# Kernel tuning notes

Measured on AMD Instinct MI355X. Metric: run time of the kernel, lower is better.

The kernel has to match this reference:

```python
import jax, jax.numpy as jnp
import numpy as np

DIM = 256
WIN = 7
HEADS = 8
N = WIN * WIN
HEAD_DIM = DIM // HEADS
SCALE = HEAD_DIM ** -0.5


def _relative_position_index():
    coords = np.stack(np.meshgrid(np.arange(WIN), np.arange(WIN), indexing='ij'))  # [2,W,W]
    cf = coords.reshape(2, -1)  # [2, N]
    rel = cf[:, :, None] - cf[:, None, :]  # [2, N, N]
    rel = rel.transpose(1, 2, 0)  # [N, N, 2]
    rel[:, :, 0] += WIN - 1
    rel[:, :, 1] += WIN - 1
    rel[:, :, 0] *= 2 * WIN - 1
    return rel.sum(-1).astype(np.int32)  # [N, N]


def setup_inputs() -> dict:
    key = jax.random.key(0)
    ks = jax.random.split(key, 8)
    B_ = 4096
    nW = 64
    x = jax.random.normal(ks[0], (B_, N, DIM), dtype=jnp.float32)
    mask = jnp.zeros((nW, N, N), dtype=jnp.float32)
    qkv_w = jax.random.normal(ks[1], (3 * DIM, DIM), dtype=jnp.float32) * (DIM ** -0.5)
    qkv_b = jnp.zeros((3 * DIM,), dtype=jnp.float32)
    proj_w = jax.random.normal(ks[2], (DIM, DIM), dtype=jnp.float32) * (DIM ** -0.5)
    proj_b = jnp.zeros((DIM,), dtype=jnp.float32)
    bias_table = jax.random.normal(ks[3], ((2 * WIN - 1) ** 2, HEADS), dtype=jnp.float32) * 0.02
    rel_index = jnp.asarray(_relative_position_index())
    return {"x": x, "mask": mask, "qkv_w": qkv_w, "qkv_b": qkv_b,
            "proj_w": proj_w, "proj_b": proj_b, "bias_table": bias_table,
            "rel_index": rel_index}


def reference(x, mask, qkv_w, qkv_b, proj_w, proj_b, bias_table, rel_index):
    B_, n, C = x.shape
    qkv = (x @ qkv_w.T + qkv_b).reshape(B_, n, 3, HEADS, HEAD_DIM)
    qkv = qkv.transpose(2, 0, 3, 1, 4)  # [3, B_, H, N, d]
    q, k, v = qkv[0], qkv[1], qkv[2]
    attn = jnp.einsum('bhnd,bhmd->bhnm', q * SCALE, k)  # [B_, H, N, N]
    # gather relative position bias: [N*N] -> [N, N, H] -> [H, N, N]
    bias = bias_table[rel_index.reshape(-1)].reshape(n, n, HEADS).transpose(2, 0, 1)
    attn = attn + bias[None]
    nW = mask.shape[0]
    attn = attn.reshape(B_ // nW, nW, HEADS, n, n) + mask[None, :, None]
    attn = jax.nn.softmax(attn.reshape(B_, HEADS, n, n), axis=-1)
    out = jnp.einsum('bhnm,bhmd->bhnd', attn, v)
    out = out.transpose(0, 2, 1, 3).reshape(B_, n, C)
    return out @ proj_w.T + proj_b
```

## Files before the change

kernel.cpp:

```cpp
#include <hip/hip_runtime.h>

#define NTOK 49
#define NW   64
#define SCALEQ 0.17677669529663687f

typedef __bf16 bf16;
typedef __bf16 bf16x8 __attribute__((ext_vector_type(8)));
typedef float  f32x4  __attribute__((ext_vector_type(4)));

#define QS_OFF   0
#define KS_OFF   15680
#define VTS_OFF  31360
#define UN_OFF   45696
#define P_STRIDE 3528
#define SMEM_ELEMS 73920
#define SMEM_BYTES (SMEM_ELEMS*2)
static_assert(SMEM_BYTES == 147840, "lds budget");

__global__ __launch_bounds__(256) void prep_kernel(
    const float* __restrict__ qkv_w, const float* __restrict__ proj_w,
    const float* __restrict__ bias_table, const int* __restrict__ rel_index,
    bf16* __restrict__ wq, bf16* __restrict__ wp, float* __restrict__ bias_full)
{
  int i = blockIdx.x * 256 + threadIdx.x;
  if (i < 768*256) wq[i] = (bf16)qkv_w[i];
  if (i < 256*256) wp[i] = (bf16)proj_w[i];
  if (i < 8*49*49) {
    int h  = i / 2401;
    int nm = i - h*2401;
    bias_full[i] = bias_table[rel_index[nm]*8 + h];
  }
}

__global__ void __launch_bounds__(512, 2)
win_attn_kernel(const float* __restrict__ x,
                const float* __restrict__ mask,
                const float* __restrict__ qkv_b,
                const float* __restrict__ proj_b,
                const bf16*  __restrict__ wq,
                const bf16*  __restrict__ wp,
                const float* __restrict__ bias_full,
                float* __restrict__ out)
{
  extern __shared__ bf16 smem[];
  const int b    = blockIdx.x;
  const int tid  = threadIdx.x;
  const int wave = tid >> 6;
  const int lane = tid & 63;
  const int quad = lane >> 4;
  const int l16  = lane & 15;
  const int w    = b & (NW - 1);

  bf16* qs  = smem + QS_OFF;
  bf16* ks  = smem + KS_OFF;
  bf16* vts = smem + VTS_OFF;
  bf16* xs  = smem + UN_OFF;
  bf16* Pb  = smem + UN_OFF + wave * P_STRIDE;

  f32x4 zero4 = {0.f, 0.f, 0.f, 0.f};

  const float* xw = x + (size_t)b * (NTOK*256);
  for (int i = tid; i < NTOK*256; i += 512) {
    int n = i >> 8, c = i & 255;
    xs[n*264 + c] = (bf16)xw[i];
  }
  for (int i = tid; i < 8*32*7; i += 512) {
    int h = i / 224, r = i - h*224;
    int dd = r / 7, mm = 49 + (r - dd*7);
    vts[(h*32 + dd)*56 + mm] = (bf16)0.0f;
  }
  __syncthreads();

  {
    bf16x8 afr[4][8];
#pragma unroll
    for (int tr = 0; tr < 4; ++tr) {
      int m = tr*16 + l16; if (m > 48) m = 48;
      const bf16* arow = xs + m*264 + quad*8;
#pragma unroll
      for (int kk = 0; kk < 8; ++kk)
        afr[tr][kk] = *(const bf16x8*)(arow + kk*32);
    }
#pragma unroll 1
    for (int tci = 0; tci < 6; ++tci) {
      int jcol = (wave*6 + tci)*16 + l16;
      const bf16* wrow = wq + jcol*256 + quad*8;
      f32x4 acc[4];
#pragma unroll
      for (int tr = 0; tr < 4; ++tr) acc[tr] = zero4;
#pragma unroll
      for (int kk = 0; kk < 8; ++kk) {
        bf16x8 bfr = *(const bf16x8*)(wrow + kk*32);
#pragma unroll
        for (int tr = 0; tr < 4; ++tr)
          acc[tr] = __builtin_amdgcn_mfma_f32_16x16x32_bf16(afr[tr][kk], bfr, acc[tr], 0,0,0);
      }
      float bj = qkv_b[jcol];
      int s  = jcol >> 8;
      int hh = (jcol >> 5) & 7;
      int dd = jcol & 31;
#pragma unroll
      for (int tr = 0; tr < 4; ++tr) {
#pragma unroll
        for (int rg = 0; rg < 4; ++rg) {
          int row = tr*16 + quad*4 + rg;
          if (row < 49) {
            float v = acc[tr][rg] + bj;
            if (s == 0)      qs[(hh*49 + row)*40 + dd] = (bf16)(v * SCALEQ);
            else if (s == 1) ks[(hh*49 + row)*40 + dd] = (bf16)v;
            else             vts[(hh*32 + dd)*56 + row] = (bf16)v;
          }
        }
      }
    }
  }
  __syncthreads();

  f32x4 O[4][2];
  {
    const int h = wave;
    const bf16* qh = qs  + h*49*40;
    const bf16* kh = ks  + h*49*40;
    const bf16* vh = vts + h*32*56;

    bf16x8 qf[4], kf[4];
#pragma unroll
    for (int t = 0; t < 4; ++t) {
      int m = t*16 + l16; if (m > 48) m = 48;
      qf[t] = *(const bf16x8*)(qh + m*40 + quad*8);
      kf[t] = *(const bf16x8*)(kh + m*40 + quad*8);
    }
    f32x4 S[4][4];
#pragma unroll
    for (int tr = 0; tr < 4; ++tr)
#pragma unroll
      for (int tc = 0; tc < 4; ++tc)
        S[tr][tc] = __builtin_amdgcn_mfma_f32_16x16x32_bf16(qf[tr], kf[tc], zero4, 0,0,0);

    const float* bh = bias_full + h*2401;
    const float* mw = mask + w*2401;
#pragma unroll
    for (int tr = 0; tr < 4; ++tr) {
#pragma unroll
      for (int rg = 0; rg < 4; ++rg) {
        int row = tr*16 + quad*4 + rg;
#pragma unroll
        for (int tc = 0; tc < 4; ++tc) {
          int col = tc*16 + l16;
          float v = S[tr][tc][rg];
          if (col >= 49) v = -1e30f;
          else if (row < 49) {
            int idx = row*49 + col;
            v += bh[idx] + mw[idx];
          }
          S[tr][tc][rg] = v;
        }
        float mx = fmaxf(fmaxf(S[tr][0][rg], S[tr][1][rg]),
                         fmaxf(S[tr][2][rg], S[tr][3][rg]));
#pragma unroll
        for (int off = 1; off < 16; off <<= 1)
          mx = fmaxf(mx, __shfl_xor(mx, off));
        float sum = 0.f;
#pragma unroll
        for (int tc = 0; tc < 4; ++tc) {
          float p = __expf(S[tr][tc][rg] - mx);
          S[tr][tc][rg] = p;
          sum += p;
        }
#pragma unroll
        for (int off = 1; off < 16; off <<= 1)
          sum += __shfl_xor(sum, off);
        float inv = 1.f / sum;
        if (row < 49) {
#pragma unroll
          for (int tc = 0; tc < 4; ++tc)
            Pb[row*72 + tc*16 + l16] = (bf16)(S[tr][tc][rg] * inv);
        }
      }
    }

#pragma unroll
    for (int tr = 0; tr < 4; ++tr) { O[tr][0] = zero4; O[tr][1] = zero4; }
#pragma unroll
    for (int kst = 0; kst < 2; ++kst) {
      int mc  = kst*32 + quad*8;
      int mcv = (mc >= 56) ? 0 : mc;
      bf16x8 vf0 = *(const bf16x8*)(vh + l16*56 + mcv);
      bf16x8 vf1 = *(const bf16x8*)(vh + (16 + l16)*56 + mcv);
#pragma unroll
      for (int tr = 0; tr < 4; ++tr) {
        int row = tr*16 + l16; if (row > 48) row = 48;
        bf16x8 pf = *(const bf16x8*)(Pb + row*72 + mc);
        O[tr][0] = __builtin_amdgcn_mfma_f32_16x16x32_bf16(pf, vf0, O[tr][0], 0,0,0);
        O[tr][1] = __builtin_amdgcn_mfma_f32_16x16x32_bf16(pf, vf1, O[tr][1], 0,0,0);
      }
    }
  }
  __syncthreads();

  bf16* ost = smem + UN_OFF;
  {
    const int h = wave;
#pragma unroll
    for (int tr = 0; tr < 4; ++tr)
#pragma unroll
      for (int rg = 0; rg < 4; ++rg) {
        int row = tr*16 + quad*4 + rg;
        if (row < 49) {
          ost[row*264 + h*32 + l16]      = (bf16)O[tr][0][rg];
          ost[row*264 + h*32 + 16 + l16] = (bf16)O[tr][1][rg];
        }
      }
  }
  __syncthreads();

  {
    bf16x8 afr[4][8];
#pragma unroll
    for (int tr = 0; tr < 4; ++tr) {
      int m = tr*16 + l16; if (m > 48) m = 48;
      const bf16* arow = ost + m*264 + quad*8;
#pragma unroll
      for (int kk = 0; kk < 8; ++kk)
        afr[tr][kk] = *(const bf16x8*)(arow + kk*32);
    }
    float* ob = out + (size_t)b * (NTOK*256);
#pragma unroll 1
    for (int tci = 0; tci < 2; ++tci) {
      int ocol = (wave*2 + tci)*16 + l16;
      const bf16* wrow = wp + ocol*256 + quad*8;
      f32x4 acc[4];
#pragma unroll
      for (int tr = 0; tr < 4; ++tr) acc[tr] = zero4;
#pragma unroll
      for (int kk = 0; kk < 8; ++kk) {
        bf16x8 bfr = *(const bf16x8*)(wrow + kk*32);
#pragma unroll
        for (int tr = 0; tr < 4; ++tr)
          acc[tr] = __builtin_amdgcn_mfma_f32_16x16x32_bf16(afr[tr][kk], bfr, acc[tr], 0,0,0);
      }
      float bj = proj_b[ocol];
#pragma unroll
      for (int tr = 0; tr < 4; ++tr)
#pragma unroll
        for (int rg = 0; rg < 4; ++rg) {
          int row = tr*16 + quad*4 + rg;
          if (row < 49) ob[row*256 + ocol] = acc[tr][rg] + bj;
        }
    }
  }
}

extern "C" void kernel_launch(void* const* d_in, const int* in_sizes, int n_in,
                              void* d_out, int out_size, void* d_ws, size_t ws_size,
                              hipStream_t stream) {
  const float* x          = (const float*)d_in[0];
  const float* mask       = (const float*)d_in[1];
  const float* qkv_w      = (const float*)d_in[2];
  const float* qkv_b      = (const float*)d_in[3];
  const float* proj_w     = (const float*)d_in[4];
  const float* proj_b     = (const float*)d_in[5];
  const float* bias_table = (const float*)d_in[6];
  const int*   rel_index  = (const int*)d_in[7];
  float* out = (float*)d_out;

  bf16*  wq        = (bf16*)d_ws;
  bf16*  wp        = wq + 768*256;
  float* bias_full = (float*)((char*)d_ws + 524288);

  prep_kernel<<<768, 256, 0, stream>>>(qkv_w, proj_w, bias_table, rel_index,
                                       wq, wp, bias_full);

  (void)hipFuncSetAttribute(reinterpret_cast<const void*>(&win_attn_kernel),
                            hipFuncAttributeMaxDynamicSharedMemorySize, SMEM_BYTES);
  win_attn_kernel<<<4096, 512, SMEM_BYTES, stream>>>(
      x, mask, qkv_b, proj_b, wq, wp, bias_full, out);
}
```

Before: 774.7 us.

## Use 1024-thread blocks, splitting attention rows across two waves per head

Launches 16 waves per window instead of 8. The QKV and projection GEMMs are redistributed so each wave handles fewer output column tiles, with A fragments reloaded per k-step rather than held in registers. Attention now uses two waves per head, each taking half the query row tiles and sharing one P buffer per head. The x load is vectorised with float4 reads and packed bf16x4 stores. The aim is more waves per CU to hide latency, since 147 KB of LDS allows only one block per CU. The cost is extra LDS reads for the A fragments and barriers that span 16 waves.

```diff
diff --git a/kernel.cpp b/kernel.cpp
--- a/kernel.cpp
+++ b/kernel.cpp
@@ -5,6 +5,7 @@
 #define SCALEQ 0.17677669529663687f
 
 typedef __bf16 bf16;
+typedef __bf16 bf16x4 __attribute__((ext_vector_type(4)));
 typedef __bf16 bf16x8 __attribute__((ext_vector_type(8)));
 typedef float  f32x4  __attribute__((ext_vector_type(4)));
 
@@ -32,7 +33,7 @@
   }
 }
 
-__global__ void __launch_bounds__(512, 2)
+__global__ void __launch_bounds__(1024)
 win_attn_kernel(const float* __restrict__ x,
                 const float* __restrict__ mask,
                 const float* __restrict__ qkv_b,
@@ -55,46 +56,53 @@
   bf16* ks  = smem + KS_OFF;
   bf16* vts = smem + VTS_OFF;
   bf16* xs  = smem + UN_OFF;
-  bf16* Pb  = smem + UN_OFF + wave * P_STRIDE;
 
   f32x4 zero4 = {0.f, 0.f, 0.f, 0.f};
 
-  const float* xw = x + (size_t)b * (NTOK*256);
-  for (int i = tid; i < NTOK*256; i += 512) {
-    int n = i >> 8, c = i & 255;
-    xs[n*264 + c] = (bf16)xw[i];
-  }
-  for (int i = tid; i < 8*32*7; i += 512) {
-    int h = i / 224, r = i - h*224;
-    int dd = r / 7, mm = 49 + (r - dd*7);
-    vts[(h*32 + dd)*56 + mm] = (bf16)0.0f;
-  }
-  __syncthreads();
-
-  {
-    bf16x8 afr[4][8];
-#pragma unroll
-    for (int tr = 0; tr < 4; ++tr) {
-      int m = tr*16 + l16; if (m > 48) m = 48;
-      const bf16* arow = xs + m*264 + quad*8;
-#pragma unroll
-      for (int kk = 0; kk < 8; ++kk)
-        afr[tr][kk] = *(const bf16x8*)(arow + kk*32);
-    }
-#pragma unroll 1
-    for (int tci = 0; tci < 6; ++tci) {
-      int jcol = (wave*6 + tci)*16 + l16;
-      const bf16* wrow = wq + jcol*256 + quad*8;
-      f32x4 acc[4];
-#pragma unroll
-      for (int tr = 0; tr < 4; ++tr) acc[tr] = zero4;
-#pragma unroll
-      for (int kk = 0; kk < 8; ++kk) {
-        bf16x8 bfr = *(const bf16x8*)(wrow + kk*32);
+  {
+    const float4* xv = (const float4*)(x + (size_t)b * (NTOK*256));
+    for (int i = tid; i < NTOK*64; i += 1024) {
+      float4 v = xv[i];
+      int n = i >> 6, c = (i & 63) * 4;
+      bf16x4 pk = {(bf16)v.x, (bf16)v.y, (bf16)v.z, (bf16)v.w};
+      *(bf16x4*)(xs + n*264 + c) = pk;
+    }
+    for (int i = tid; i < 8*32*7; i += 1024) {
+      int h = i / 224, r = i - h*224;
+      int dd = r / 7, mm = 49 + (r - dd*7);
+      vts[(h*32 + dd)*56 + mm] = (bf16)0.0f;
+    }
+  }
+  __syncthreads();
+
+  {
+    f32x4 acc[3][4];
+#pragma unroll
+    for (int t = 0; t < 3; ++t)
+#pragma unroll
+      for (int tr = 0; tr < 4; ++tr) acc[t][tr] = zero4;
+
+    int jc0 = (wave*3)*16 + l16;
+    const bf16* w0 = wq + (size_t)jc0*256 + quad*8;
+#pragma unroll
+    for (int kk = 0; kk < 8; ++kk) {
+      bf16x8 afr[4];
+#pragma unroll
+      for (int tr = 0; tr < 4; ++tr) {
+        int m = tr*16 + l16; if (m > 48) m = 48;
+        afr[tr] = *(const bf16x8*)(xs + m*264 + quad*8 + kk*32);
+      }
+#pragma unroll
+      for (int t = 0; t < 3; ++t) {
+        bf16x8 bfr = *(const bf16x8*)(w0 + (size_t)t*16*256 + kk*32);
 #pragma unroll
         for (int tr = 0; tr < 4; ++tr)
-          acc[tr] = __builtin_amdgcn_mfma_f32_16x16x32_bf16(afr[tr][kk], bfr, acc[tr], 0,0,0);
-      }
+          acc[t][tr] = __builtin_amdgcn_mfma_f32_16x16x32_bf16(afr[tr], bfr, acc[t][tr], 0,0,0);
+      }
+    }
+#pragma unroll
+    for (int t = 0; t < 3; ++t) {
+      int jcol = (wave*3 + t)*16 + l16;
       float bj = qkv_b[jcol];
       int s  = jcol >> 8;
       int hh = (jcol >> 5) & 7;
@@ -105,7 +113,7 @@
         for (int rg = 0; rg < 4; ++rg) {
           int row = tr*16 + quad*4 + rg;
           if (row < 49) {
-            float v = acc[tr][rg] + bj;
+            float v = acc[t][tr][rg] + bj;
             if (s == 0)      qs[(hh*49 + row)*40 + dd] = (bf16)(v * SCALEQ);
             else if (s == 1) ks[(hh*49 + row)*40 + dd] = (bf16)v;
             else             vts[(hh*32 + dd)*56 + row] = (bf16)v;
@@ -116,23 +124,29 @@
   }
   __syncthreads();
 
-  f32x4 O[4][2];
-  {
-    const int h = wave;
+  f32x4 O[2][2];
+  {
+    const int h    = wave >> 1;
+    const int half = wave & 1;
     const bf16* qh = qs  + h*49*40;
     const bf16* kh = ks  + h*49*40;
     const bf16* vh = vts + h*32*56;
-
-    bf16x8 qf[4], kf[4];
+    bf16* Pb = smem + UN_OFF + h * P_STRIDE;
+
+    bf16x8 qf[2], kf[4];
+#pragma unroll
+    for (int t = 0; t < 2; ++t) {
+      int m = (half*2 + t)*16 + l16; if (m > 48) m = 48;
+      qf[t] = *(const bf16x8*)(qh + m*40 + quad*8);
+    }
 #pragma unroll
     for (int t = 0; t < 4; ++t) {
       int m = t*16 + l16; if (m > 48) m = 48;
-      qf[t] = *(const bf16x8*)(qh + m*40 + quad*8);
       kf[t] = *(const bf16x8*)(kh + m*40 + quad*8);
     }
-    f32x4 S[4][4];
-#pragma unroll
-    for (int tr = 0; tr < 4; ++tr)
+    f32x4 S[2][4];
+#pragma unroll
+    for (int tr = 0; tr < 2; ++tr)
 #pragma unroll
       for (int tc = 0; tc < 4; ++tc)
         S[tr][tc] = __builtin_amdgcn_mfma_f32_16x16x32_bf16(qf[tr], kf[tc], zero4, 0,0,0);
@@ -140,31 +154,32 @@
     const float* bh = bias_full + h*2401;
     const float* mw = mask + w*2401;
 #pragma unroll
-    for (int tr = 0; tr < 4; ++tr) {
+    for (int tr2 = 0; tr2 < 2; ++tr2) {
+      int tr = half*2 + tr2;
 #pragma unroll
       for (int rg = 0; rg < 4; ++rg) {
         int row = tr*16 + quad*4 + rg;
 #pragma unroll
         for (int tc = 0; tc < 4; ++tc) {
           int col = tc*16 + l16;
-          float v = S[tr][tc][rg];
+          float v = S[tr2][tc][rg];
           if (col >= 49) v = -1e30f;
           else if (row < 49) {
             int idx = row*49 + col;
             v += bh[idx] + mw[idx];
           }
-          S[tr][tc][rg] = v;
-        }
-        float mx = fmaxf(fmaxf(S[tr][0][rg], S[tr][1][rg]),
-                         fmaxf(S[tr][2][rg], S[tr][3][rg]));
+          S[tr2][tc][rg] = v;
+        }
+        float mx = fmaxf(fmaxf(S[tr2][0][rg], S[tr2][1][rg]),
+                         fmaxf(S[tr2][2][rg], S[tr2][3][rg]));
 #pragma unroll
         for (int off = 1; off < 16; off <<= 1)
           mx = fmaxf(mx, __shfl_xor(mx, off));
         float sum = 0.f;
 #pragma unroll
         for (int tc = 0; tc < 4; ++tc) {
-          float p = __expf(S[tr][tc][rg] - mx);
-          S[tr][tc][rg] = p;
+          float p = __expf(S[tr2][tc][rg] - mx);
+          S[tr2][tc][rg] = p;
           sum += p;
         }
 #pragma unroll
@@ -174,13 +189,13 @@
         if (row < 49) {
 #pragma unroll
           for (int tc = 0; tc < 4; ++tc)
-            Pb[row*72 + tc*16 + l16] = (bf16)(S[tr][tc][rg] * inv);
-        }
-      }
-    }
-
-#pragma unroll
-    for (int tr = 0; tr < 4; ++tr) { O[tr][0] = zero4; O[tr][1] = zero4; }
+            Pb[row*72 + tc*16 + l16] = (bf16)(S[tr2][tc][rg] * inv);
+        }
+      }
+    }
+
+#pragma unroll
+    for (int tr = 0; tr < 2; ++tr) { O[tr][0] = zero4; O[tr][1] = zero4; }
 #pragma unroll
     for (int kst = 0; kst < 2; ++kst) {
       int mc  = kst*32 + quad*8;
@@ -188,66 +203,58 @@
       bf16x8 vf0 = *(const bf16x8*)(vh + l16*56 + mcv);
       bf16x8 vf1 = *(const bf16x8*)(vh + (16 + l16)*56 + mcv);
 #pragma unroll
+      for (int tr2 = 0; tr2 < 2; ++tr2) {
+        int row = (half*2 + tr2)*16 + l16; if (row > 48) row = 48;
+        bf16x8 pf = *(const bf16x8*)(Pb + row*72 + mc);
+        O[tr2][0] = __builtin_amdgcn_mfma_f32_16x16x32_bf16(pf, vf0, O[tr2][0], 0,0,0);
+        O[tr2][1] = __builtin_amdgcn_mfma_f32_16x16x32_bf16(pf, vf1, O[tr2][1], 0,0,0);
+      }
+    }
+  }
+  __syncthreads();
+
+  bf16* ost = smem + UN_OFF;
+  {
+    const int h    = wave >> 1;
+    const int half = wave & 1;
+#pragma unroll
+    for (int tr2 = 0; tr2 < 2; ++tr2)
+#pragma unroll
+      for (int rg = 0; rg < 4; ++rg) {
+        int row = (half*2 + tr2)*16 + quad*4 + rg;
+        if (row < 49) {
+          ost[row*264 + h*32 + l16]      = (bf16)O[tr2][0][rg];
+          ost[row*264 + h*32 + 16 + l16] = (bf16)O[tr2][1][rg];
+        }
+      }
+  }
+  __syncthreads();
+
+  {
+    f32x4 acc[4];
+#pragma unroll
+    for (int tr = 0; tr < 4; ++tr) acc[tr] = zero4;
+    int ocol = wave*16 + l16;
+    const bf16* wrow = wp + (size_t)ocol*256 + quad*8;
+#pragma unroll
+    for (int kk = 0; kk < 8; ++kk) {
+      bf16x8 bfr = *(const bf16x8*)(wrow + kk*32);
+#pragma unroll
       for (int tr = 0; tr < 4; ++tr) {
-        int row = tr*16 + l16; if (row > 48) row = 48;
-        bf16x8 pf = *(const bf16x8*)(Pb + row*72 + mc);
-        O[tr][0] = __builtin_amdgcn_mfma_f32_16x16x32_bf16(pf, vf0, O[tr][0], 0,0,0);
-        O[tr][1] = __builtin_amdgcn_mfma_f32_16x16x32_bf16(pf, vf1, O[tr][1], 0,0,0);
-      }
-    }
-  }
-  __syncthreads();
-
-  bf16* ost = smem + UN_OFF;
-  {
-    const int h = wave;
+        int m = tr*16 + l16; if (m > 48) m = 48;
+        bf16x8 afr = *(const bf16x8*)(ost + m*264 + quad*8 + kk*32);
+        acc[tr] = __builtin_amdgcn_mfma_f32_16x16x32_bf16(afr, bfr, acc[tr], 0,0,0);
+      }
+    }
+    float bj = proj_b[ocol];
+    float* ob = out + (size_t)b * (NTOK*256);
 #pragma unroll
     for (int tr = 0; tr < 4; ++tr)
 #pragma unroll
       for (int rg = 0; rg < 4; ++rg) {
         int row = tr*16 + quad*4 + rg;
-        if (row < 49) {
-          ost[row*264 + h*32 + l16]      = (bf16)O[tr][0][rg];
-          ost[row*264 + h*32 + 16 + l16] = (bf16)O[tr][1][rg];
-        }
-      }
-  }
-  __syncthreads();
-
-  {
-    bf16x8 afr[4][8];
-#pragma unroll
-    for (int tr = 0; tr < 4; ++tr) {
-      int m = tr*16 + l16; if (m > 48) m = 48;
-      const bf16* arow = ost + m*264 + quad*8;
-#pragma unroll
-      for (int kk = 0; kk < 8; ++kk)
-        afr[tr][kk] = *(const bf16x8*)(arow + kk*32);
-    }
-    float* ob = out + (size_t)b * (NTOK*256);
-#pragma unroll 1
-    for (int tci = 0; tci < 2; ++tci) {
-      int ocol = (wave*2 + tci)*16 + l16;
-      const bf16* wrow = wp + ocol*256 + quad*8;
-      f32x4 acc[4];
-#pragma unroll
-      for (int tr = 0; tr < 4; ++tr) acc[tr] = zero4;
-#pragma unroll
-      for (int kk = 0; kk < 8; ++kk) {
-        bf16x8 bfr = *(const bf16x8*)(wrow + kk*32);
-#pragma unroll
-        for (int tr = 0; tr < 4; ++tr)
-          acc[tr] = __builtin_amdgcn_mfma_f32_16x16x32_bf16(afr[tr][kk], bfr, acc[tr], 0,0,0);
-      }
-      float bj = proj_b[ocol];
-#pragma unroll
-      for (int tr = 0; tr < 4; ++tr)
-#pragma unroll
-        for (int rg = 0; rg < 4; ++rg) {
-          int row = tr*16 + quad*4 + rg;
-          if (row < 49) ob[row*256 + ocol] = acc[tr][rg] + bj;
-        }
-    }
+        if (row < 49) ob[row*256 + ocol] = acc[tr][rg] + bj;
+      }
   }
 }
 
@@ -273,6 +280,6 @@
 
   (void)hipFuncSetAttribute(reinterpret_cast<const void*>(&win_attn_kernel),
                             hipFuncAttributeMaxDynamicSharedMemorySize, SMEM_BYTES);
-  win_attn_kernel<<<4096, 512, SMEM_BYTES, stream>>>(
+  win_attn_kernel<<<4096, 1024, SMEM_BYTES, stream>>>(
       x, mask, qkv_b, proj_b, wq, wp, bias_full, out);
 }
```

Result: faster. 738.0 us (-4.7%).
